# Kernel optimization log

Measured on AMD Instinct MI355X. Metric: run time of the kernel, lower is better.

## Reference

```python
import jax, jax.numpy as jnp
import numpy as np

B, T, N, C = 1, 2, 10000, 64
H, Co = 4, 64
E = 160000
NEG_SLOPE = 0.2
LN_EPS = 1e-5


def setup_inputs() -> dict:
    key = jax.random.key(0)
    ks = jax.random.split(key, 8)
    s_in = 1.0 / np.sqrt(C)
    s_att = 1.0 / np.sqrt(Co)
    s_proj = 1.0 / np.sqrt(H * Co)
    return {
        "x": jax.random.normal(ks[0], (B, T, N, C), jnp.float32),
        "edge_index": jax.random.randint(ks[1], (2, E), 0, N, dtype=jnp.int32),
        "W_l": jax.random.normal(ks[2], (C, H * Co), jnp.float32) * s_in,
        "b_l": jnp.zeros((H * Co,), jnp.float32),
        "W_r": jax.random.normal(ks[3], (C, H * Co), jnp.float32) * s_in,
        "b_r": jnp.zeros((H * Co,), jnp.float32),
        "att": jax.random.normal(ks[4], (H, Co), jnp.float32) * s_att,
        "bias": jnp.zeros((H * Co,), jnp.float32),
        "W_proj": jax.random.normal(ks[5], (H * Co, Co), jnp.float32) * s_proj,
        "b_proj": jnp.zeros((Co,), jnp.float32),
        "ln_gamma": jnp.ones((Co,), jnp.float32),
        "ln_beta": jnp.zeros((Co,), jnp.float32),
    }


def reference(x, edge_index, W_l, b_l, W_r, b_r, att, bias, W_proj, b_proj, ln_gamma, ln_beta):
    src, dst = edge_index[0], edge_index[1]
    # node transforms: [B,T,N,H,Co]
    x_l = (x @ W_l + b_l).reshape(B, T, N, H, Co)
    x_r = (x @ W_r + b_r).reshape(B, T, N, H, Co)
    # per-edge gathers: [B,T,E,H,Co]
    x_j = x_l[:, :, src]  # source-side features (messages)
    x_i = x_r[:, :, dst]  # target-side features
    m = jax.nn.leaky_relu(x_i + x_j, NEG_SLOPE)
    alpha = jnp.einsum('bteho,ho->bteh', m, att)  # [B,T,E,H]
    # segment softmax over edges grouped by target node (edge axis leading)
    a = jnp.moveaxis(alpha, 2, 0)  # [E,B,T,H]
    amax = jax.lax.stop_gradient(jax.ops.segment_max(a, dst, num_segments=N))
    a = jnp.exp(a - amax[dst])
    denom = jax.ops.segment_sum(a, dst, num_segments=N)
    attn = a / denom[dst]  # [E,B,T,H]
    # weighted messages scattered to target nodes
    msg = jnp.moveaxis(x_j, 2, 0) * attn[..., None]  # [E,B,T,H,Co]
    agg = jax.ops.segment_sum(msg, dst, num_segments=N)  # [N,B,T,H,Co]
    out = jnp.moveaxis(agg, 0, 2).reshape(B, T, N, H * Co) + bias
    x_mha = jax.nn.relu(out)
    # projection + identity residual (in_channels == out_channels)
    x_sam = x_mha @ W_proj + b_proj + x
    mu = jnp.mean(x_sam, axis=-1, keepdims=True)
    var = jnp.var(x_sam, axis=-1, keepdims=True)
    y = (x_sam - mu) * jax.lax.rsqrt(var + LN_EPS) * ln_gamma + ln_beta
    return jax.nn.relu(y)
```

## Files before the change

kernel.cpp:

```cpp
#include <hip/hip_runtime.h>

#define T_  2
#define N_  10000
#define C_  64
#define H_  4
#define Co_ 64
#define E_  160000
#define HC_ 256
#define PAD_ 48
#define NEG_SLOPE 0.2f
#define LN_EPS 1e-5f
#define SCAT_BLOCKS (E_ / 256)
#define GEMM_BLOCKS (T_ * N_ / 32)

typedef float v2f __attribute__((ext_vector_type(2)));

#if __has_builtin(__builtin_elementwise_fma)
#define PKFMA(a, b, c) __builtin_elementwise_fma((a), (b), (c))
#else
#define PKFMA(a, b, c) ((a) * (b) + (c))
#endif

__device__ __forceinline__ v2f v2(float x, float y) { v2f r; r.x = x; r.y = y; return r; }
__device__ __forceinline__ v2f sp(float x) { v2f r; r.x = x; r.y = x; return r; }

__device__ __forceinline__ float bf2f(unsigned short u) {
    return __uint_as_float((unsigned)u << 16);
}
__device__ __forceinline__ unsigned short f2bf(float f) {
    const unsigned u = __float_as_uint(f);
    return (unsigned short)((u + 0x7FFFu + ((u >> 16) & 1u)) >> 16);
}
__device__ __forceinline__ float4 u2f4(ushort4 u) {
    return make_float4(bf2f(u.x), bf2f(u.y), bf2f(u.z), bf2f(u.w));
}

__device__ __forceinline__ void red16x4(float& p0, float& p1, float& p2, float& p3) {
    asm("s_nop 1\n\t"
        "v_add_f32_dpp %0, %0, %0 quad_perm:[1,0,3,2] row_mask:0xf bank_mask:0xf\n\t"
        "v_add_f32_dpp %1, %1, %1 quad_perm:[1,0,3,2] row_mask:0xf bank_mask:0xf\n\t"
        "v_add_f32_dpp %2, %2, %2 quad_perm:[1,0,3,2] row_mask:0xf bank_mask:0xf\n\t"
        "v_add_f32_dpp %3, %3, %3 quad_perm:[1,0,3,2] row_mask:0xf bank_mask:0xf\n\t"
        "v_add_f32_dpp %0, %0, %0 quad_perm:[2,3,0,1] row_mask:0xf bank_mask:0xf\n\t"
        "v_add_f32_dpp %1, %1, %1 quad_perm:[2,3,0,1] row_mask:0xf bank_mask:0xf\n\t"
        "v_add_f32_dpp %2, %2, %2 quad_perm:[2,3,0,1] row_mask:0xf bank_mask:0xf\n\t"
        "v_add_f32_dpp %3, %3, %3 quad_perm:[2,3,0,1] row_mask:0xf bank_mask:0xf\n\t"
        "v_add_f32_dpp %0, %0, %0 row_half_mirror row_mask:0xf bank_mask:0xf\n\t"
        "v_add_f32_dpp %1, %1, %1 row_half_mirror row_mask:0xf bank_mask:0xf\n\t"
        "v_add_f32_dpp %2, %2, %2 row_half_mirror row_mask:0xf bank_mask:0xf\n\t"
        "v_add_f32_dpp %3, %3, %3 row_half_mirror row_mask:0xf bank_mask:0xf\n\t"
        "v_add_f32_dpp %0, %0, %0 row_mirror row_mask:0xf bank_mask:0xf\n\t"
        "v_add_f32_dpp %1, %1, %1 row_mirror row_mask:0xf bank_mask:0xf\n\t"
        "v_add_f32_dpp %2, %2, %2 row_mirror row_mask:0xf bank_mask:0xf\n\t"
        "v_add_f32_dpp %3, %3, %3 row_mirror row_mask:0xf bank_mask:0xf"
        : "+v"(p0), "+v"(p1), "+v"(p2), "+v"(p3));
}

__device__ __forceinline__ float edot2(const v2f xa, const v2f xb,
                                       const v2f aa, const v2f ab, const float4 c) {
    v2f u = v2(c.x, c.y) + xa;
    v2f v = v2(c.z, c.w) + xb;
    v2f lu = __builtin_elementwise_max(u, u * 0.2f);
    v2f lv = __builtin_elementwise_max(v, v * 0.2f);
    v2f p = PKFMA(lv, ab, lu * aa);
    return p.x + p.y;
}

__device__ __forceinline__ void group_update(
        const v2f xa, const v2f xb, const v2f aa, const v2f ab,
        const float4 c0, const float4 c1, const float4 c2, const float4 c3,
        int k, int cnt, float& m, float& s, float4& acc) {
    float p0 = edot2(xa, xb, aa, ab, c0);
    float p1 = edot2(xa, xb, aa, ab, c1);
    float p2 = edot2(xa, xb, aa, ab, c2);
    float p3 = edot2(xa, xb, aa, ab, c3);
    red16x4(p0, p1, p2, p3);
    if (k + 1 >= cnt) p1 = -INFINITY;
    if (k + 2 >= cnt) p2 = -INFINITY;
    if (k + 3 >= cnt) p3 = -INFINITY;
    const float gm = fmaxf(fmaxf(p0, p1), fmaxf(p2, p3));
    const float mn = fmaxf(m, gm);
    const float sc = __expf(m - mn);
    const float w0 = __expf(p0 - mn);
    const float w1 = __expf(p1 - mn);
    const float w2 = __expf(p2 - mn);
    const float w3 = __expf(p3 - mn);
    s = fmaf(s, sc, w0 + w1 + w2 + w3);
    v2f q01 = v2(c3.x, c3.y) * w3;
    q01 = PKFMA(v2(c2.x, c2.y), sp(w2), q01);
    q01 = PKFMA(v2(c1.x, c1.y), sp(w1), q01);
    q01 = PKFMA(v2(c0.x, c0.y), sp(w0), q01);
    v2f r01 = PKFMA(v2(acc.x, acc.y), sp(sc), q01);
    v2f q23 = v2(c3.z, c3.w) * w3;
    q23 = PKFMA(v2(c2.z, c2.w), sp(w2), q23);
    q23 = PKFMA(v2(c1.z, c1.w), sp(w1), q23);
    q23 = PKFMA(v2(c0.z, c0.w), sp(w0), q23);
    v2f r23 = PKFMA(v2(acc.z, acc.w), sp(sc), q23);
    acc.x = r01.x; acc.y = r01.y; acc.z = r23.x; acc.w = r23.y;
    m = mn;
}

__global__ __launch_bounds__(256) void scat_gemm(
        const int* __restrict__ src, const int* __restrict__ dst,
        int* __restrict__ cursor, unsigned short* __restrict__ perm,
        const float* __restrict__ x, const float* __restrict__ Wl,
        const float* __restrict__ bl, const float* __restrict__ Wr,
        const float* __restrict__ br, unsigned short* __restrict__ xlb,
        float* __restrict__ xr) {
    __shared__ float4 xs[32 * 16];
    const int tid = threadIdx.x;
    if (blockIdx.x < SCAT_BLOCKS) {
        const int e = blockIdx.x * 256 + tid;
        const int d = dst[e];
        const int pos = atomicAdd(&cursor[d], 1);
        if (pos < PAD_) perm[d * PAD_ + pos] = (unsigned short)src[e];
        return;
    }
    const int r0 = (blockIdx.x - SCAT_BLOCKS) * 32;
    xs[tid]       = ((const float4*)(x + (size_t)r0 * C_))[tid];
    xs[256 + tid] = ((const float4*)(x + (size_t)r0 * C_))[256 + tid];
    __syncthreads();

    const int wv    = tid >> 6;
    const int mat   = wv >> 1;
    const int rbase = (wv & 1) << 4;
    const int col4  = tid & 63;
    const float* W  = mat ? Wr : Wl;
    const float4 b4 = ((const float4*)(mat ? br : bl))[col4];

    v2f accA[16], accB[16];
    #pragma unroll
    for (int r = 0; r < 16; ++r) { accA[r] = v2(b4.x, b4.y); accB[r] = v2(b4.z, b4.w); }

    #pragma unroll 2
    for (int c4 = 0; c4 < 16; ++c4) {
        const float4 w0 = ((const float4*)(W + (size_t)(c4 * 4 + 0) * HC_))[col4];
        const float4 w1 = ((const float4*)(W + (size_t)(c4 * 4 + 1) * HC_))[col4];
        const float4 w2 = ((const float4*)(W + (size_t)(c4 * 4 + 2) * HC_))[col4];
        const float4 w3 = ((const float4*)(W + (size_t)(c4 * 4 + 3) * HC_))[col4];
        const v2f w0A = v2(w0.x, w0.y), w0B = v2(w0.z, w0.w);
        const v2f w1A = v2(w1.x, w1.y), w1B = v2(w1.z, w1.w);
        const v2f w2A = v2(w2.x, w2.y), w2B = v2(w2.z, w2.w);
        const v2f w3A = v2(w3.x, w3.y), w3B = v2(w3.z, w3.w);
        #pragma unroll
        for (int r = 0; r < 16; ++r) {
            const float4 xv = xs[(rbase + r) * 16 + c4];
            accA[r] = PKFMA(sp(xv.x), w0A, accA[r]);
            accB[r] = PKFMA(sp(xv.x), w0B, accB[r]);
            accA[r] = PKFMA(sp(xv.y), w1A, accA[r]);
            accB[r] = PKFMA(sp(xv.y), w1B, accB[r]);
            accA[r] = PKFMA(sp(xv.z), w2A, accA[r]);
            accB[r] = PKFMA(sp(xv.z), w2B, accB[r]);
            accA[r] = PKFMA(sp(xv.w), w3A, accA[r]);
            accB[r] = PKFMA(sp(xv.w), w3B, accB[r]);
        }
    }
    if (mat) {
        #pragma unroll
        for (int r = 0; r < 16; ++r) {
            float4 o4;
            o4.x = accA[r].x; o4.y = accA[r].y; o4.z = accB[r].x; o4.w = accB[r].y;
            ((float4*)(xr + (size_t)(r0 + rbase + r) * HC_))[col4] = o4;
        }
    } else {
        #pragma unroll
        for (int r = 0; r < 16; ++r) {
            ushort4 u;
            u.x = f2bf(accA[r].x); u.y = f2bf(accA[r].y);
            u.z = f2bf(accB[r].x); u.w = f2bf(accB[r].y);
            ((ushort4*)(xlb + (size_t)(r0 + rbase + r) * HC_))[col4] = u;
        }
    }
}

__global__ __launch_bounds__(128, 6) void node_proj(
        const unsigned short* __restrict__ xlb, const float* __restrict__ xr,
        const float* __restrict__ att, const unsigned short* __restrict__ perm,
        const int* __restrict__ cursor, const float* __restrict__ bias,
        const float* __restrict__ Wp, const float* __restrict__ bp,
        const float* __restrict__ x, const float* __restrict__ gamma,
        const float* __restrict__ beta, float* __restrict__ out) {
    __shared__ float sh_act[T_][HC_];
    __shared__ float sh_part[T_][T_][Co_];
    const int t    = threadIdx.x >> 6;
    const int lane = threadIdx.x & 63;
    const int n    = blockIdx.x;
    const int deg  = min(cursor[n], PAD_);
    const float4 av = ((const float4*)att)[lane];
    const float4 xi = ((const float4*)&xr[((size_t)t * N_ + n) * HC_])[lane];
    const int myidx = (lane < deg) ? (int)perm[n * PAD_ + lane] : 0;
    const unsigned short* xlt = xlb + (size_t)t * N_ * HC_;

    const v2f xa = v2(xi.x, xi.y), xb = v2(xi.z, xi.w);
    const v2f aa = v2(av.x, av.y), ab = v2(av.z, av.w);

    float m = -INFINITY, s = 0.f;
    float4 acc = make_float4(0.f, 0.f, 0.f, 0.f);

    ushort4 A0, A1, A2, A3, B0, B1, B2, B3;
    auto fetchA = [&](int kk) {
        const int i0 = __builtin_amdgcn_readlane(myidx, kk + 0);
        const int i1 = __builtin_amdgcn_readlane(myidx, kk + 1);
        const int i2 = __builtin_amdgcn_readlane(myidx, kk + 2);
        const int i3 = __builtin_amdgcn_readlane(myidx, kk + 3);
        A0 = ((const ushort4*)&xlt[(size_t)i0 * HC_])[lane];
        A1 = ((const ushort4*)&xlt[(size_t)i1 * HC_])[lane];
        A2 = ((const ushort4*)&xlt[(size_t)i2 * HC_])[lane];
        A3 = ((const ushort4*)&xlt[(size_t)i3 * HC_])[lane];
    };
    auto fetchB = [&](int kk) {
        const int i0 = __builtin_amdgcn_readlane(myidx, kk + 0);
        const int i1 = __builtin_amdgcn_readlane(myidx, kk + 1);
        const int i2 = __builtin_amdgcn_readlane(myidx, kk + 2);
        const int i3 = __builtin_amdgcn_readlane(myidx, kk + 3);
        B0 = ((const ushort4*)&xlt[(size_t)i0 * HC_])[lane];
        B1 = ((const ushort4*)&xlt[(size_t)i1 * HC_])[lane];
        B2 = ((const ushort4*)&xlt[(size_t)i2 * HC_])[lane];
        B3 = ((const ushort4*)&xlt[(size_t)i3 * HC_])[lane];
    };
    if (deg > 0) fetchA(0);
    if (deg > 4) fetchB(4);
    for (int k = 0; k < deg; k += 8) {
        {
            const float4 c0 = u2f4(A0), c1 = u2f4(A1), c2 = u2f4(A2), c3 = u2f4(A3);
            if (k + 8 < deg) fetchA(k + 8);
            group_update(xa, xb, aa, ab, c0, c1, c2, c3, k, deg, m, s, acc);
        }
        if (k + 4 < deg) {
            const float4 c0 = u2f4(B0), c1 = u2f4(B1), c2 = u2f4(B2), c3 = u2f4(B3);
            if (k + 12 < deg) fetchB(k + 12);
            group_update(xa, xb, aa, ab, c0, c1, c2, c3, k + 4, deg, m, s, acc);
        }
    }

    {
        const float4 bias4 = ((const float4*)bias)[lane];
        const float inv = (deg > 0) ? 1.f / s : 0.f;
        float4 v;
        v.x = fmaxf(fmaf(acc.x, inv, bias4.x), 0.f);
        v.y = fmaxf(fmaf(acc.y, inv, bias4.y), 0.f);
        v.z = fmaxf(fmaf(acc.z, inv, bias4.z), 0.f);
        v.w = fmaxf(fmaf(acc.w, inv, bias4.w), 0.f);
        ((float4*)&sh_act[t][0])[lane] = v;
    }
    __syncthreads();

    v2f P0 = v2(0.f, 0.f), P1 = v2(0.f, 0.f);
    {
        const int kq = t * 32;
        #pragma unroll 4
        for (int k4 = 0; k4 < 32; ++k4) {
            const int k = (kq + k4) * 4;
            const float w0 = Wp[(size_t)(k + 0) * Co_ + lane];
            const float w1 = Wp[(size_t)(k + 1) * Co_ + lane];
            const float w2 = Wp[(size_t)(k + 2) * Co_ + lane];
            const float w3 = Wp[(size_t)(k + 3) * Co_ + lane];
            const v2f w01 = v2(w0, w1), w23 = v2(w2, w3);
            const float4 a0 = ((const float4*)&sh_act[0][0])[kq + k4];
            const float4 a1 = ((const float4*)&sh_act[1][0])[kq + k4];
            P0 = PKFMA(v2(a0.x, a0.y), w01, P0);
            P0 = PKFMA(v2(a0.z, a0.w), w23, P0);
            P1 = PKFMA(v2(a1.x, a1.y), w01, P1);
            P1 = PKFMA(v2(a1.z, a1.w), w23, P1);
        }
    }
    sh_part[t][0][lane] = P0.x + P0.y;
    sh_part[t][1][lane] = P1.x + P1.y;
    __syncthreads();

    const int o = lane;
    float p = sh_part[0][t][o] + sh_part[1][t][o]
            + bp[o] + x[((size_t)t * N_ + n) * C_ + o];
    const float go = gamma[o], bo = beta[o];
    float s1r = p;
    #pragma unroll
    for (int off = 1; off < 64; off <<= 1) s1r += __shfl_xor(s1r, off, 64);
    const float mu = s1r * (1.f / 64.f);
    const float dv = p - mu;
    float s2r = dv * dv;
    #pragma unroll
    for (int off = 1; off < 64; off <<= 1) s2r += __shfl_xor(s2r, off, 64);
    out[((size_t)t * N_ + n) * C_ + o] =
        fmaxf(dv * rsqrtf(s2r * (1.f / 64.f) + LN_EPS) * go + bo, 0.f);
}

extern "C" void kernel_launch(void* const* d_in, const int* in_sizes, int n_in,
                              void* d_out, int out_size, void* d_ws, size_t ws_size,
                              hipStream_t stream) {
    const float* x    = (const float*)d_in[0];
    const int*   ei   = (const int*)  d_in[1];
    const float* Wl   = (const float*)d_in[2];
    const float* bl   = (const float*)d_in[3];
    const float* Wr   = (const float*)d_in[4];
    const float* br   = (const float*)d_in[5];
    const float* att  = (const float*)d_in[6];
    const float* bias = (const float*)d_in[7];
    const float* Wp   = (const float*)d_in[8];
    const float* bp   = (const float*)d_in[9];
    const float* gam  = (const float*)d_in[10];
    const float* bet  = (const float*)d_in[11];
    const int* src = ei;
    const int* dst = ei + E_;

    char* ws = (char*)d_ws;
    unsigned short* xlb  = (unsigned short*)ws;
    float*          xr   = (float*)(xlb + (size_t)T_ * N_ * HC_);
    int*            cursor = (int*)(xr + (size_t)T_ * N_ * HC_);
    unsigned short* perm   = (unsigned short*)(cursor + N_);

    hipMemsetAsync(cursor, 0, N_ * sizeof(int), stream);
    scat_gemm<<<SCAT_BLOCKS + GEMM_BLOCKS, 256, 0, stream>>>(
        src, dst, cursor, perm, x, Wl, bl, Wr, br, xlb, xr);
    node_proj<<<N_, 128, 0, stream>>>(xlb, xr, att, perm, cursor, bias,
                                      Wp, bp, x, gam, bet, (float*)d_out);
}
```

Measured before the change: 161.0 us.

## Split wave into two edge halves with 16-byte bf16 gathers and drop online max

The edge-attention loop is remapped so each half-wave handles a different edge. Each lane now loads 8 bf16 channels with one 16-byte load, so the per-head dot-product reduction spans 8 lanes (three DPP steps) instead of 16. The online-softmax running max and rescaling are removed: logits are pre-scaled by log2(e) through the attention vector and exponentiated directly with exp2f. The two halves' partial sums are then combined with cross-half shuffles. This cuts ALU, DPP and exp work per edge, but skipping max subtraction risks overflow if logits grow large, and the final cross-half reduction adds some cost.

```diff
diff --git a/kernel.cpp b/kernel.cpp
--- a/kernel.cpp
+++ b/kernel.cpp
@@ -14,6 +14,7 @@
 #define GEMM_BLOCKS (T_ * N_ / 32)
 
 typedef float v2f __attribute__((ext_vector_type(2)));
+typedef unsigned short bfx8 __attribute__((ext_vector_type(8)));
 
 #if __has_builtin(__builtin_elementwise_fma)
 #define PKFMA(a, b, c) __builtin_elementwise_fma((a), (b), (c))
@@ -31,73 +32,18 @@
     const unsigned u = __float_as_uint(f);
     return (unsigned short)((u + 0x7FFFu + ((u >> 16) & 1u)) >> 16);
 }
-__device__ __forceinline__ float4 u2f4(ushort4 u) {
-    return make_float4(bf2f(u.x), bf2f(u.y), bf2f(u.z), bf2f(u.w));
-}
-
-__device__ __forceinline__ void red16x4(float& p0, float& p1, float& p2, float& p3) {
+
+__device__ __forceinline__ void red8x2(float& p0, float& p1) {
     asm("s_nop 1\n\t"
         "v_add_f32_dpp %0, %0, %0 quad_perm:[1,0,3,2] row_mask:0xf bank_mask:0xf\n\t"
         "v_add_f32_dpp %1, %1, %1 quad_perm:[1,0,3,2] row_mask:0xf bank_mask:0xf\n\t"
-        "v_add_f32_dpp %2, %2, %2 quad_perm:[1,0,3,2] row_mask:0xf bank_mask:0xf\n\t"
-        "v_add_f32_dpp %3, %3, %3 quad_perm:[1,0,3,2] row_mask:0xf bank_mask:0xf\n\t"
+        "s_nop 0\n\t"
         "v_add_f32_dpp %0, %0, %0 quad_perm:[2,3,0,1] row_mask:0xf bank_mask:0xf\n\t"
         "v_add_f32_dpp %1, %1, %1 quad_perm:[2,3,0,1] row_mask:0xf bank_mask:0xf\n\t"
-        "v_add_f32_dpp %2, %2, %2 quad_perm:[2,3,0,1] row_mask:0xf bank_mask:0xf\n\t"
-        "v_add_f32_dpp %3, %3, %3 quad_perm:[2,3,0,1] row_mask:0xf bank_mask:0xf\n\t"
+        "s_nop 0\n\t"
         "v_add_f32_dpp %0, %0, %0 row_half_mirror row_mask:0xf bank_mask:0xf\n\t"
-        "v_add_f32_dpp %1, %1, %1 row_half_mirror row_mask:0xf bank_mask:0xf\n\t"
-        "v_add_f32_dpp %2, %2, %2 row_half_mirror row_mask:0xf bank_mask:0xf\n\t"
-        "v_add_f32_dpp %3, %3, %3 row_half_mirror row_mask:0xf bank_mask:0xf\n\t"
-        "v_add_f32_dpp %0, %0, %0 row_mirror row_mask:0xf bank_mask:0xf\n\t"
-        "v_add_f32_dpp %1, %1, %1 row_mirror row_mask:0xf bank_mask:0xf\n\t"
-        "v_add_f32_dpp %2, %2, %2 row_mirror row_mask:0xf bank_mask:0xf\n\t"
-        "v_add_f32_dpp %3, %3, %3 row_mirror row_mask:0xf bank_mask:0xf"
-        : "+v"(p0), "+v"(p1), "+v"(p2), "+v"(p3));
-}
-
-__device__ __forceinline__ float edot2(const v2f xa, const v2f xb,
-                                       const v2f aa, const v2f ab, const float4 c) {
-    v2f u = v2(c.x, c.y) + xa;
-    v2f v = v2(c.z, c.w) + xb;
-    v2f lu = __builtin_elementwise_max(u, u * 0.2f);
-    v2f lv = __builtin_elementwise_max(v, v * 0.2f);
-    v2f p = PKFMA(lv, ab, lu * aa);
-    return p.x + p.y;
-}
-
-__device__ __forceinline__ void group_update(
-        const v2f xa, const v2f xb, const v2f aa, const v2f ab,
-        const float4 c0, const float4 c1, const float4 c2, const float4 c3,
-        int k, int cnt, float& m, float& s, float4& acc) {
-    float p0 = edot2(xa, xb, aa, ab, c0);
-    float p1 = edot2(xa, xb, aa, ab, c1);
-    float p2 = edot2(xa, xb, aa, ab, c2);
-    float p3 = edot2(xa, xb, aa, ab, c3);
-    red16x4(p0, p1, p2, p3);
-    if (k + 1 >= cnt) p1 = -INFINITY;
-    if (k + 2 >= cnt) p2 = -INFINITY;
-    if (k + 3 >= cnt) p3 = -INFINITY;
-    const float gm = fmaxf(fmaxf(p0, p1), fmaxf(p2, p3));
-    const float mn = fmaxf(m, gm);
-    const float sc = __expf(m - mn);
-    const float w0 = __expf(p0 - mn);
-    const float w1 = __expf(p1 - mn);
-    const float w2 = __expf(p2 - mn);
-    const float w3 = __expf(p3 - mn);
-    s = fmaf(s, sc, w0 + w1 + w2 + w3);
-    v2f q01 = v2(c3.x, c3.y) * w3;
-    q01 = PKFMA(v2(c2.x, c2.y), sp(w2), q01);
-    q01 = PKFMA(v2(c1.x, c1.y), sp(w1), q01);
-    q01 = PKFMA(v2(c0.x, c0.y), sp(w0), q01);
-    v2f r01 = PKFMA(v2(acc.x, acc.y), sp(sc), q01);
-    v2f q23 = v2(c3.z, c3.w) * w3;
-    q23 = PKFMA(v2(c2.z, c2.w), sp(w2), q23);
-    q23 = PKFMA(v2(c1.z, c1.w), sp(w1), q23);
-    q23 = PKFMA(v2(c0.z, c0.w), sp(w0), q23);
-    v2f r23 = PKFMA(v2(acc.z, acc.w), sp(sc), q23);
-    acc.x = r01.x; acc.y = r01.y; acc.z = r23.x; acc.w = r23.y;
-    m = mn;
+        "v_add_f32_dpp %1, %1, %1 row_half_mirror row_mask:0xf bank_mask:0xf"
+        : "+v"(p0), "+v"(p1));
 }
 
 __global__ __launch_bounds__(256) void scat_gemm(
@@ -184,64 +130,117 @@
     __shared__ float sh_part[T_][T_][Co_];
     const int t    = threadIdx.x >> 6;
     const int lane = threadIdx.x & 63;
+    const int q    = lane & 31;
+    const int half = lane >> 5;
     const int n    = blockIdx.x;
     const int deg  = min(cursor[n], PAD_);
-    const float4 av = ((const float4*)att)[lane];
-    const float4 xi = ((const float4*)&xr[((size_t)t * N_ + n) * HC_])[lane];
+    const int lim  = deg - half;
+    const size_t row = (size_t)t * N_ + n;
+
+    const float4 xiA = ((const float4*)&xr[row * HC_])[2 * q];
+    const float4 xiB = ((const float4*)&xr[row * HC_])[2 * q + 1];
+    const float4 avA = ((const float4*)att)[2 * q];
+    const float4 avB = ((const float4*)att)[2 * q + 1];
+    const v2f X0 = v2(xiA.x, xiA.y), X1 = v2(xiA.z, xiA.w);
+    const v2f X2 = v2(xiB.x, xiB.y), X3 = v2(xiB.z, xiB.w);
+    const float L2E = 1.44269504f;
+    const v2f A0v = v2(avA.x * L2E, avA.y * L2E), A1v = v2(avA.z * L2E, avA.w * L2E);
+    const v2f A2v = v2(avB.x * L2E, avB.y * L2E), A3v = v2(avB.z * L2E, avB.w * L2E);
+
     const int myidx = (lane < deg) ? (int)perm[n * PAD_ + lane] : 0;
     const unsigned short* xlt = xlb + (size_t)t * N_ * HC_;
 
-    const v2f xa = v2(xi.x, xi.y), xb = v2(xi.z, xi.w);
-    const v2f aa = v2(av.x, av.y), ab = v2(av.z, av.w);
-
-    float m = -INFINITY, s = 0.f;
-    float4 acc = make_float4(0.f, 0.f, 0.f, 0.f);
-
-    ushort4 A0, A1, A2, A3, B0, B1, B2, B3;
+    float s = 0.f;
+    v2f ac0 = v2(0.f, 0.f), ac1 = ac0, ac2 = ac0, ac3 = ac0;
+
+    bfx8 Au, Bu, Cu, Du;
     auto fetchA = [&](int kk) {
         const int i0 = __builtin_amdgcn_readlane(myidx, kk + 0);
         const int i1 = __builtin_amdgcn_readlane(myidx, kk + 1);
         const int i2 = __builtin_amdgcn_readlane(myidx, kk + 2);
         const int i3 = __builtin_amdgcn_readlane(myidx, kk + 3);
-        A0 = ((const ushort4*)&xlt[(size_t)i0 * HC_])[lane];
-        A1 = ((const ushort4*)&xlt[(size_t)i1 * HC_])[lane];
-        A2 = ((const ushort4*)&xlt[(size_t)i2 * HC_])[lane];
-        A3 = ((const ushort4*)&xlt[(size_t)i3 * HC_])[lane];
+        const int ia = half ? i1 : i0;
+        const int ib = half ? i3 : i2;
+        Au = *(const bfx8*)&xlt[(size_t)ia * HC_ + 8 * q];
+        Bu = *(const bfx8*)&xlt[(size_t)ib * HC_ + 8 * q];
     };
     auto fetchB = [&](int kk) {
         const int i0 = __builtin_amdgcn_readlane(myidx, kk + 0);
         const int i1 = __builtin_amdgcn_readlane(myidx, kk + 1);
         const int i2 = __builtin_amdgcn_readlane(myidx, kk + 2);
         const int i3 = __builtin_amdgcn_readlane(myidx, kk + 3);
-        B0 = ((const ushort4*)&xlt[(size_t)i0 * HC_])[lane];
-        B1 = ((const ushort4*)&xlt[(size_t)i1 * HC_])[lane];
-        B2 = ((const ushort4*)&xlt[(size_t)i2 * HC_])[lane];
-        B3 = ((const ushort4*)&xlt[(size_t)i3 * HC_])[lane];
+        const int ia = half ? i1 : i0;
+        const int ib = half ? i3 : i2;
+        Cu = *(const bfx8*)&xlt[(size_t)ia * HC_ + 8 * q];
+        Du = *(const bfx8*)&xlt[(size_t)ib * HC_ + 8 * q];
+    };
+    auto pair_update = [&](const bfx8 u0, const bfx8 u1, int kbase) {
+        const v2f c00 = v2(bf2f(u0[0]), bf2f(u0[1]));
+        const v2f c01 = v2(bf2f(u0[2]), bf2f(u0[3]));
+        const v2f c02 = v2(bf2f(u0[4]), bf2f(u0[5]));
+        const v2f c03 = v2(bf2f(u0[6]), bf2f(u0[7]));
+        const v2f c10 = v2(bf2f(u1[0]), bf2f(u1[1]));
+        const v2f c11 = v2(bf2f(u1[2]), bf2f(u1[3]));
+        const v2f c12 = v2(bf2f(u1[4]), bf2f(u1[5]));
+        const v2f c13 = v2(bf2f(u1[6]), bf2f(u1[7]));
+        v2f u, l, P;
+        u = c00 + X0; l = __builtin_elementwise_max(u, u * NEG_SLOPE); P = l * A0v;
+        u = c01 + X1; l = __builtin_elementwise_max(u, u * NEG_SLOPE); P = PKFMA(l, A1v, P);
+        u = c02 + X2; l = __builtin_elementwise_max(u, u * NEG_SLOPE); P = PKFMA(l, A2v, P);
+        u = c03 + X3; l = __builtin_elementwise_max(u, u * NEG_SLOPE); P = PKFMA(l, A3v, P);
+        float p0 = P.x + P.y;
+        u = c10 + X0; l = __builtin_elementwise_max(u, u * NEG_SLOPE); P = l * A0v;
+        u = c11 + X1; l = __builtin_elementwise_max(u, u * NEG_SLOPE); P = PKFMA(l, A1v, P);
+        u = c12 + X2; l = __builtin_elementwise_max(u, u * NEG_SLOPE); P = PKFMA(l, A2v, P);
+        u = c13 + X3; l = __builtin_elementwise_max(u, u * NEG_SLOPE); P = PKFMA(l, A3v, P);
+        float p1 = P.x + P.y;
+        p0 = (kbase < lim)     ? p0 : -INFINITY;
+        p1 = (kbase + 2 < lim) ? p1 : -INFINITY;
+        red8x2(p0, p1);
+        const float w0 = exp2f(p0);
+        const float w1 = exp2f(p1);
+        s += w0 + w1;
+        ac0 = PKFMA(c00, sp(w0), ac0); ac0 = PKFMA(c10, sp(w1), ac0);
+        ac1 = PKFMA(c01, sp(w0), ac1); ac1 = PKFMA(c11, sp(w1), ac1);
+        ac2 = PKFMA(c02, sp(w0), ac2); ac2 = PKFMA(c12, sp(w1), ac2);
+        ac3 = PKFMA(c03, sp(w0), ac3); ac3 = PKFMA(c13, sp(w1), ac3);
     };
     if (deg > 0) fetchA(0);
     if (deg > 4) fetchB(4);
     for (int k = 0; k < deg; k += 8) {
         {
-            const float4 c0 = u2f4(A0), c1 = u2f4(A1), c2 = u2f4(A2), c3 = u2f4(A3);
+            const bfx8 u0 = Au, u1 = Bu;
             if (k + 8 < deg) fetchA(k + 8);
-            group_update(xa, xb, aa, ab, c0, c1, c2, c3, k, deg, m, s, acc);
+            pair_update(u0, u1, k);
         }
         if (k + 4 < deg) {
-            const float4 c0 = u2f4(B0), c1 = u2f4(B1), c2 = u2f4(B2), c3 = u2f4(B3);
+            const bfx8 u0 = Cu, u1 = Du;
             if (k + 12 < deg) fetchB(k + 12);
-            group_update(xa, xb, aa, ab, c0, c1, c2, c3, k + 4, deg, m, s, acc);
-        }
-    }
-
-    {
-        const float4 bias4 = ((const float4*)bias)[lane];
+            pair_update(u0, u1, k + 4);
+        }
+    }
+
+    s += __shfl_xor(s, 32, 64);
+    ac0.x += __shfl_xor(ac0.x, 32, 64); ac0.y += __shfl_xor(ac0.y, 32, 64);
+    ac1.x += __shfl_xor(ac1.x, 32, 64); ac1.y += __shfl_xor(ac1.y, 32, 64);
+    ac2.x += __shfl_xor(ac2.x, 32, 64); ac2.y += __shfl_xor(ac2.y, 32, 64);
+    ac3.x += __shfl_xor(ac3.x, 32, 64); ac3.y += __shfl_xor(ac3.y, 32, 64);
+
+    if (lane < 32) {
         const float inv = (deg > 0) ? 1.f / s : 0.f;
-        float4 v;
-        v.x = fmaxf(fmaf(acc.x, inv, bias4.x), 0.f);
-        v.y = fmaxf(fmaf(acc.y, inv, bias4.y), 0.f);
-        v.z = fmaxf(fmaf(acc.z, inv, bias4.z), 0.f);
-        v.w = fmaxf(fmaf(acc.w, inv, bias4.w), 0.f);
-        ((float4*)&sh_act[t][0])[lane] = v;
+        const float4 bA = ((const float4*)bias)[2 * q];
+        const float4 bB = ((const float4*)bias)[2 * q + 1];
+        float4 vA, vB;
+        vA.x = fmaxf(fmaf(ac0.x, inv, bA.x), 0.f);
+        vA.y = fmaxf(fmaf(ac0.y, inv, bA.y), 0.f);
+        vA.z = fmaxf(fmaf(ac1.x, inv, bA.z), 0.f);
+        vA.w = fmaxf(fmaf(ac1.y, inv, bA.w), 0.f);
+        vB.x = fmaxf(fmaf(ac2.x, inv, bB.x), 0.f);
+        vB.y = fmaxf(fmaf(ac2.y, inv, bB.y), 0.f);
+        vB.z = fmaxf(fmaf(ac3.x, inv, bB.z), 0.f);
+        vB.w = fmaxf(fmaf(ac3.y, inv, bB.w), 0.f);
+        ((float4*)&sh_act[t][0])[2 * q]     = vA;
+        ((float4*)&sh_act[t][0])[2 * q + 1] = vB;
     }
     __syncthreads();
 
```

Measured after the change: 158.9 us (median of 2 runs). Within noise of the previous version (-1.3%).
